# Performance work log

Hardware: AMD Instinct MI355X
Metric: run time of the kernel (lower is better)

Reference implementation:

```python
import jax, jax.numpy as jnp
import numpy as np

N = 100000          # nodes
E = 3200000         # edges
C_IN = 64
HIDDEN = 64
NUM_CLASSES = 10
NUM_GRAPHS = 256
EPS = 1e-5


def _graph_conv(x, src, dst, w_rel, w_root, b):
    # PyG GraphConv(aggr='mean'): out_i = W_rel * mean_{j->i} x_j + W_root * x_i + b
    msg_sum = jax.ops.segment_sum(x[src], dst, num_segments=N)            # [N, C]
    cnt = jax.ops.segment_sum(jnp.ones((src.shape[0], 1), x.dtype), dst,
                              num_segments=N)                             # [N, 1]
    agg = msg_sum / jnp.maximum(cnt, 1.0)
    return agg @ w_rel + x @ w_root + b


def _batch_norm(x, gamma, beta):
    # PyG BatchNorm in training mode: batch stats over the node dimension
    mean = jnp.mean(x, axis=0)
    var = jnp.var(x, axis=0)
    return (x - mean) * jax.lax.rsqrt(var + EPS) * gamma + beta


def setup_inputs() -> dict:
    key = jax.random.key(0)
    ks = jax.random.split(key, 20)
    x = jax.random.normal(ks[0], (N, C_IN), dtype=jnp.float32)
    edge_index = jax.random.randint(ks[1], (2, E), 0, N, dtype=jnp.int32)
    batch = jnp.sort(jax.random.randint(ks[2], (N,), 0, NUM_GRAPHS, dtype=jnp.int32))

    def lin(k, fan_in, fan_out):
        s = 1.0 / np.sqrt(fan_in)
        return jax.random.uniform(k, (fan_in, fan_out), jnp.float32, -s, s)

    dims = [(C_IN, 16), (16, 32), (32, 32), (32, HIDDEN)]
    params = {}
    ki = 3
    for i, (ci, co) in enumerate(dims, start=1):
        params[f"w_rel{i}"] = lin(ks[ki], ci, co); ki += 1
        params[f"w_root{i}"] = lin(ks[ki], ci, co); ki += 1
        params[f"b{i}"] = jnp.zeros((co,), jnp.float32)
        params[f"g{i}"] = jnp.ones((co,), jnp.float32)
        params[f"be{i}"] = jnp.zeros((co,), jnp.float32)
    params["w_lin1"] = lin(ks[ki], HIDDEN, HIDDEN); ki += 1
    params["b_lin1"] = jnp.zeros((HIDDEN,), jnp.float32)
    params["w_lin2"] = lin(ks[ki], HIDDEN, NUM_CLASSES); ki += 1
    params["b_lin2"] = jnp.zeros((NUM_CLASSES,), jnp.float32)

    return {"x": x, "edge_index": edge_index, "batch": batch, **params}


def reference(x, edge_index, batch,
              w_rel1, w_root1, b1, g1, be1,
              w_rel2, w_root2, b2, g2, be2,
              w_rel3, w_root3, b3, g3, be3,
              w_rel4, w_root4, b4, g4, be4,
              w_lin1, b_lin1, w_lin2, b_lin2):
    src, dst = edge_index[0], edge_index[1]
    h = jax.nn.elu(_batch_norm(_graph_conv(x, src, dst, w_rel1, w_root1, b1), g1, be1))
    h = jax.nn.elu(_batch_norm(_graph_conv(h, src, dst, w_rel2, w_root2, b2), g2, be2))
    h = jax.nn.elu(_batch_norm(_graph_conv(h, src, dst, w_rel3, w_root3, b3), g3, be3))
    h = jax.nn.elu(_batch_norm(_graph_conv(h, src, dst, w_rel4, w_root4, b4), g4, be4))
    # global mean pool over graphs
    pooled = jax.ops.segment_sum(h, batch, num_segments=NUM_GRAPHS)
    cnt = jax.ops.segment_sum(jnp.ones((N, 1), h.dtype), batch, num_segments=NUM_GRAPHS)
    pooled = pooled / jnp.maximum(cnt, 1.0)
    z = jax.nn.relu(pooled @ w_lin1 + b_lin1)
    # dropout omitted (deterministic / eval mode)
    logits = z @ w_lin2 + b_lin2
    return jax.nn.log_softmax(logits, axis=-1)
```

## Files before the change

### kernel.cpp

```cpp
#include <hip/hip_runtime.h>
#include <hip/hip_bf16.h>
#include <math.h>

#define NGRAPHS 256
#define BSHIFT 7
#define NBUCK 1024
#define NSORT 64
#define SBLK 256
#define SMASK 0x01FFFFFFu

__global__ __launch_bounds__(1024) void k_bhist(const int* __restrict__ dst, int* __restrict__ hmat, int E) {
    __shared__ int hist[NBUCK];
    for (int i = threadIdx.x; i < NBUCK; i += 1024) hist[i] = 0;
    __syncthreads();
    int chunk = (E + NSORT - 1) / NSORT;
    int lo = blockIdx.x * chunk;
    int hi = lo + chunk; if (hi > E) hi = E;
    for (int i = lo + threadIdx.x; i < hi; i += 1024) {
        int d = __builtin_nontemporal_load(dst + i);
        atomicAdd(&hist[d >> BSHIFT], 1);
    }
    __syncthreads();
    for (int i = threadIdx.x; i < NBUCK; i += 1024)
        hmat[(size_t)blockIdx.x * NBUCK + i] = hist[i];
}

__global__ __launch_bounds__(256) void k_cscan(int* __restrict__ hmat, int* __restrict__ btot) {
    int col = blockIdx.x * 256 + threadIdx.x;
    int run = 0;
#pragma unroll 4
    for (int r = 0; r < NSORT; r++) {
        int v = hmat[(size_t)r * NBUCK + col];
        hmat[(size_t)r * NBUCK + col] = run;
        run += v;
    }
    btot[col] = run;
}

__global__ __launch_bounds__(1024) void k_bscan(const int* __restrict__ btot, int* __restrict__ bstart) {
    __shared__ int s[1024];
    int tid = threadIdx.x;
    int v = btot[tid];
    s[tid] = v;
    __syncthreads();
    for (int off = 1; off < 1024; off <<= 1) {
        int t = (tid >= off) ? s[tid - off] : 0;
        __syncthreads();
        s[tid] += t;
        __syncthreads();
    }
    bstart[tid] = s[tid] - v;
    if (tid == 1023) bstart[NBUCK] = s[1023];
}

__global__ __launch_bounds__(1024) void k_bscatter(const int* __restrict__ src, const int* __restrict__ dst,
                                                   const int* __restrict__ hmat, const int* __restrict__ bstart,
                                                   unsigned* __restrict__ ebuf, int E) {
    __shared__ int cur[NBUCK];
    for (int i = threadIdx.x; i < NBUCK; i += 1024)
        cur[i] = bstart[i] + hmat[(size_t)blockIdx.x * NBUCK + i];
    __syncthreads();
    int chunk = (E + NSORT - 1) / NSORT;
    int lo = blockIdx.x * chunk;
    int hi = lo + chunk; if (hi > E) hi = E;
    for (int i = lo + threadIdx.x; i < hi; i += 1024) {
        int d = __builtin_nontemporal_load(dst + i);
        int s = __builtin_nontemporal_load(src + i);
        int p = atomicAdd(&cur[d >> BSHIFT], 1);
        ebuf[p] = (unsigned)s | ((unsigned)(d & 127) << 25);
    }
}

__global__ __launch_bounds__(256) void k_sort2(const unsigned* __restrict__ ebuf, const int* __restrict__ bstart,
                                               int* __restrict__ csr, int* __restrict__ row_start, int N) {
    __shared__ int hist[128];
    __shared__ int sc[128];
    __shared__ int scur[128];
    int b = blockIdx.x;
    int e0 = bstart[b], e1 = bstart[b + 1];
    if (threadIdx.x < 128) hist[threadIdx.x] = 0;
    __syncthreads();
    for (int i = e0 + threadIdx.x; i < e1; i += 256)
        atomicAdd(&hist[__builtin_nontemporal_load(ebuf + i) >> 25], 1);
    __syncthreads();
    if (threadIdx.x < 128) sc[threadIdx.x] = hist[threadIdx.x];
    __syncthreads();
    for (int off = 1; off < 128; off <<= 1) {
        int t = 0;
        if (threadIdx.x < 128 && threadIdx.x >= off) t = sc[threadIdx.x - off];
        __syncthreads();
        if (threadIdx.x < 128) sc[threadIdx.x] += t;
        __syncthreads();
    }
    if (threadIdx.x < 128) {
        int inc = sc[threadIdx.x];
        int ex = inc - hist[threadIdx.x];
        scur[threadIdx.x] = e0 + ex;
        int node = (b << BSHIFT) + threadIdx.x;
        if (node < N) row_start[node] = e0 + ex;
        if (node == N - 1) row_start[N] = e0 + inc;
    }
    __syncthreads();
    for (int i = e0 + threadIdx.x; i < e1; i += 256) {
        unsigned w = __builtin_nontemporal_load(ebuf + i);
        int p = atomicAdd(&scur[w >> 25], 1);
        csr[p] = (int)(w & SMASK);
    }
}

template <int CI, int CO, bool HAS_REL, bool HAS_ROOT, bool ADD_AGG, bool HAS_BIAS>
__global__ __launch_bounds__(256) void k_lin(const float* __restrict__ hroot, const float* __restrict__ hrel,
                                             const float* __restrict__ w_rel, const float* __restrict__ w_root,
                                             const float* __restrict__ bias, const float* __restrict__ aggadd,
                                             float* __restrict__ out, int N) {
    constexpr int QPR = CO / 4;
    __shared__ float s_rel[HAS_REL ? CI * CO : 1];
    __shared__ float s_root[HAS_ROOT ? CI * CO : 1];
    __shared__ float s_b[HAS_BIAS ? CO : 4];
    if (HAS_REL)
        for (int i = threadIdx.x; i < CI * CO; i += 256) s_rel[i] = w_rel[i];
    if (HAS_ROOT)
        for (int i = threadIdx.x; i < CI * CO; i += 256) s_root[i] = w_root[i];
    if (HAS_BIAS && threadIdx.x < CO) s_b[threadIdx.x] = bias[threadIdx.x];
    __syncthreads();

    int t = blockIdx.x * 256 + threadIdx.x;
    int n = t / QPR;
    int c0 = (t % QPR) * 4;
    if (n >= N) return;

    float rr[HAS_ROOT ? CI : 1];
    if (HAS_ROOT) {
        const float4* hp = (const float4*)(hroot + (size_t)n * CI);
#pragma unroll
        for (int i = 0; i < CI / 4; i++) {
            float4 v = hp[i];
            rr[4 * i + 0] = v.x; rr[4 * i + 1] = v.y; rr[4 * i + 2] = v.z; rr[4 * i + 3] = v.w;
        }
    }
    float ar[HAS_REL ? CI : 1];
    if (HAS_REL) {
        const float4* mp = (const float4*)(hrel + (size_t)n * CI);
#pragma unroll
        for (int i = 0; i < CI / 4; i++) {
            float4 v = mp[i];
            ar[4 * i + 0] = v.x; ar[4 * i + 1] = v.y; ar[4 * i + 2] = v.z; ar[4 * i + 3] = v.w;
        }
    }

    float4 acc;
    if (HAS_BIAS) acc = *(const float4*)&s_b[c0];
    else { acc.x = 0.f; acc.y = 0.f; acc.z = 0.f; acc.w = 0.f; }
    if (ADD_AGG) {
        float4 v = *(const float4*)(aggadd + (size_t)n * CO + c0);
        acc.x += v.x; acc.y += v.y; acc.z += v.z; acc.w += v.w;
    }

#pragma unroll
    for (int ci = 0; ci < CI; ci++) {
        if (HAS_REL) {
            float a = ar[ci];
            float4 w = *(const float4*)&s_rel[ci * CO + c0];
            acc.x += a * w.x; acc.y += a * w.y; acc.z += a * w.z; acc.w += a * w.w;
        }
        if (HAS_ROOT) {
            float hv = rr[ci];
            float4 w = *(const float4*)&s_root[ci * CO + c0];
            acc.x += hv * w.x; acc.y += hv * w.y; acc.z += hv * w.z; acc.w += hv * w.w;
        }
    }
    *(float4*)(out + (size_t)n * CO + c0) = acc;
}

template <int C>
__global__ __launch_bounds__(256) void k_gather(const float* __restrict__ h, const int* __restrict__ row_start,
                                                const int* __restrict__ csr, float* __restrict__ agg, int N) {
    constexpr int LPR = C / 4;
    constexpr int EPP = 64 / LPR;
    int lane = threadIdx.x & 63;
    int wid = blockIdx.x * 4 + (threadIdx.x >> 6);
    if (wid >= N) return;
    int r0 = row_start[wid];
    int deg = row_start[wid + 1] - r0;
    int es = lane / LPR;
    int cq = (lane % LPR) * 4;
    float ax = 0.f, ay = 0.f, az = 0.f, aw = 0.f;
    for (int j0 = 0; j0 < deg; j0 += 4 * EPP) {
        int s[4]; bool p[4];
#pragma unroll
        for (int u = 0; u < 4; u++) {
            int j = j0 + u * EPP + es;
            p[u] = j < deg;
            s[u] = __builtin_nontemporal_load(&csr[r0 + (p[u] ? j : 0)]);
        }
#pragma unroll
        for (int u = 0; u < 4; u++) {
            float4 v = *(const float4*)(h + (size_t)s[u] * C + cq);
            if (p[u]) { ax += v.x; ay += v.y; az += v.z; aw += v.w; }
        }
    }
#pragma unroll
    for (int off = LPR; off < 64; off <<= 1) {
        ax += __shfl_xor(ax, off, 64);
        ay += __shfl_xor(ay, off, 64);
        az += __shfl_xor(az, off, 64);
        aw += __shfl_xor(aw, off, 64);
    }
    if (lane < LPR) {
        float rec = 1.0f / (float)(deg > 0 ? deg : 1);
        float4 o; o.x = ax * rec; o.y = ay * rec; o.z = az * rec; o.w = aw * rec;
        *(float4*)(agg + (size_t)wid * C + cq) = o;
    }
}

template <int CO>
__global__ __launch_bounds__(256) void k_stats(const float* __restrict__ h, float* __restrict__ partials, int N) {
    constexpr int QPR = CO / 4;
    int total = N * QPR;
    float s0 = 0, s1 = 0, s2 = 0, s3 = 0, q0 = 0, q1 = 0, q2 = 0, q3 = 0;
    int idx = blockIdx.x * 256 + threadIdx.x;
    for (int i = idx; i < total; i += SBLK * 256) {
        float4 v = ((const float4*)h)[i];
        s0 += v.x; q0 += v.x * v.x;
        s1 += v.y; q1 += v.y * v.y;
        s2 += v.z; q2 += v.z * v.z;
        s3 += v.w; q3 += v.w * v.w;
    }
#pragma unroll
    for (int off = QPR; off < 64; off <<= 1) {
        s0 += __shfl_xor(s0, off, 64); q0 += __shfl_xor(q0, off, 64);
        s1 += __shfl_xor(s1, off, 64); q1 += __shfl_xor(q1, off, 64);
        s2 += __shfl_xor(s2, off, 64); q2 += __shfl_xor(q2, off, 64);
        s3 += __shfl_xor(s3, off, 64); q3 += __shfl_xor(q3, off, 64);
    }
    __shared__ float part[4][2 * CO];
    int lane = threadIdx.x & 63;
    int w = threadIdx.x >> 6;
    if (lane < QPR) {
        int cq = lane * 4;
        part[w][cq + 0] = s0; part[w][CO + cq + 0] = q0;
        part[w][cq + 1] = s1; part[w][CO + cq + 1] = q1;
        part[w][cq + 2] = s2; part[w][CO + cq + 2] = q2;
        part[w][cq + 3] = s3; part[w][CO + cq + 3] = q3;
    }
    __syncthreads();
    if (threadIdx.x < 2 * CO) {
        float v = part[0][threadIdx.x] + part[1][threadIdx.x] + part[2][threadIdx.x] + part[3][threadIdx.x];
        partials[blockIdx.x * (2 * CO) + threadIdx.x] = v;
    }
}

__global__ __launch_bounds__(128) void k_sfinal(const float* __restrict__ partials, const float* __restrict__ g,
                                                const float* __restrict__ be, float* __restrict__ stats,
                                                int CO, float invN) {
    __shared__ float red[128];
    int c = threadIdx.x;
    float s = 0.f;
    if (c < 2 * CO) {
        for (int b = 0; b < SBLK; b++) s += partials[b * 2 * CO + c];
    }
    red[c] = s;
    __syncthreads();
    if (c < CO) {
        float mean = red[c] * invN;
        float var = red[CO + c] * invN - mean * mean;
        float sc = g[c] * rsqrtf(var + 1e-5f);
        stats[128 + c] = sc;
        stats[192 + c] = be[c] - mean * sc;
    }
}

template <int CO>
__global__ __launch_bounds__(256) void k_bn_elu(float* __restrict__ h, const float* __restrict__ stats, int N) {
    __shared__ float sc[CO], sh[CO];
    if (threadIdx.x < CO) {
        sc[threadIdx.x] = stats[128 + threadIdx.x];
        sh[threadIdx.x] = stats[192 + threadIdx.x];
    }
    __syncthreads();
    int total = N * (CO / 4);
    int i = blockIdx.x * 256 + threadIdx.x;
    if (i >= total) return;
    float4 v = ((float4*)h)[i];
    int cq = (i % (CO / 4)) * 4;
    v.x = v.x * sc[cq + 0] + sh[cq + 0];
    v.y = v.y * sc[cq + 1] + sh[cq + 1];
    v.z = v.z * sc[cq + 2] + sh[cq + 2];
    v.w = v.w * sc[cq + 3] + sh[cq + 3];
    v.x = v.x > 0.f ? v.x : expm1f(v.x);
    v.y = v.y > 0.f ? v.y : expm1f(v.y);
    v.z = v.z > 0.f ? v.z : expm1f(v.z);
    v.w = v.w > 0.f ? v.w : expm1f(v.w);
    ((float4*)h)[i] = v;
}

__global__ __launch_bounds__(256) void k_pool(const float* __restrict__ h, const int* __restrict__ batch,
                                              float* __restrict__ pooled, float* __restrict__ cntg, int N) {
    int lane = threadIdx.x & 63;
    int wid = blockIdx.x * 4 + (threadIdx.x >> 6);
    int n0 = wid * 64;
    if (n0 >= N) return;
    int nmax = N - n0; if (nmax > 64) nmax = 64;
    int cur = batch[n0];
    float acc = 0.f;
    int run = 0;
    for (int k = 0; k < nmax; k++) {
        int g = batch[n0 + k];
        if (g != cur) {
            atomicAdd(&pooled[(size_t)cur * 64 + lane], acc);
            if (lane == 0) atomicAdd(&cntg[cur], (float)run);
            cur = g; acc = 0.f; run = 0;
        }
        acc += h[(size_t)(n0 + k) * 64 + lane];
        run++;
    }
    atomicAdd(&pooled[(size_t)cur * 64 + lane], acc);
    if (lane == 0) atomicAdd(&cntg[cur], (float)run);
}

__global__ __launch_bounds__(256) void k_head(const float* __restrict__ pooled, const float* __restrict__ cntg,
                                              const float* __restrict__ w1, const float* __restrict__ b1,
                                              const float* __restrict__ w2, const float* __restrict__ b2,
                                              float* __restrict__ out) {
    int g = threadIdx.x;
    float rec = 1.0f / fmaxf(cntg[g], 1.0f);
    float p[64];
    {
        const float4* pp = (const float4*)(pooled + (size_t)g * 64);
#pragma unroll
        for (int i = 0; i < 16; i++) {
            float4 v = pp[i];
            p[4 * i + 0] = v.x * rec; p[4 * i + 1] = v.y * rec;
            p[4 * i + 2] = v.z * rec; p[4 * i + 3] = v.w * rec;
        }
    }
    float lg[10];
#pragma unroll
    for (int t = 0; t < 10; t++) lg[t] = b2[t];
#pragma unroll 1
    for (int j = 0; j < 64; j++) {
        float a = b1[j];
#pragma unroll
        for (int k = 0; k < 64; k++) a += p[k] * w1[k * 64 + j];
        a = fmaxf(a, 0.f);
#pragma unroll
        for (int t = 0; t < 10; t++) lg[t] += a * w2[j * 10 + t];
    }
    float m = -1e30f;
#pragma unroll
    for (int t = 0; t < 10; t++) m = fmaxf(m, lg[t]);
    float s = 0.f;
#pragma unroll
    for (int t = 0; t < 10; t++) s += expf(lg[t] - m);
    float lse = m + logf(s);
#pragma unroll
    for (int t = 0; t < 10; t++) out[(size_t)g * 10 + t] = lg[t] - lse;
}

extern "C" void kernel_launch(void* const* d_in, const int* in_sizes, int n_in,
                              void* d_out, int out_size, void* d_ws, size_t ws_size,
                              hipStream_t stream) {
    const float* x = (const float*)d_in[0];
    const int* ei = (const int*)d_in[1];
    const int* batch = (const int*)d_in[2];
    const int N = in_sizes[0] / 64;
    const int E = in_sizes[1] / 2;
    const int* src = ei;
    const int* dst = ei + E;

    const float* w_rel1 = (const float*)d_in[3];
    const float* w_root1 = (const float*)d_in[4];
    const float* b1 = (const float*)d_in[5];
    const float* g1 = (const float*)d_in[6];
    const float* be1 = (const float*)d_in[7];
    const float* w_rel2 = (const float*)d_in[8];
    const float* w_root2 = (const float*)d_in[9];
    const float* b2 = (const float*)d_in[10];
    const float* g2 = (const float*)d_in[11];
    const float* be2 = (const float*)d_in[12];
    const float* w_rel3 = (const float*)d_in[13];
    const float* w_root3 = (const float*)d_in[14];
    const float* b3 = (const float*)d_in[15];
    const float* g3 = (const float*)d_in[16];
    const float* be3 = (const float*)d_in[17];
    const float* w_rel4 = (const float*)d_in[18];
    const float* w_root4 = (const float*)d_in[19];
    const float* b4 = (const float*)d_in[20];
    const float* g4 = (const float*)d_in[21];
    const float* be4 = (const float*)d_in[22];
    const float* w_lin1 = (const float*)d_in[23];
    const float* b_lin1 = (const float*)d_in[24];
    const float* w_lin2 = (const float*)d_in[25];
    const float* b_lin2 = (const float*)d_in[26];

    char* ws = (char*)d_ws;
    size_t off = 0;
    auto alloc = [&](size_t bytes) { size_t o = off; off += (bytes + 255) & ~(size_t)255; return o; };
    int* hmat = (int*)(ws + alloc((size_t)NSORT * NBUCK * 4));
    int* btot = (int*)(ws + alloc((size_t)NBUCK * 4));
    int* bstart = (int*)(ws + alloc((size_t)(NBUCK + 1) * 4));
    unsigned* ebuf = (unsigned*)(ws + alloc((size_t)E * 4));
    int* csr = (int*)(ws + alloc((size_t)E * 4));
    int* row_start = (int*)(ws + alloc((size_t)(N + 1) * 4));
    float* agg = (float*)(ws + alloc((size_t)N * 32 * 4));
    float* y1 = (float*)(ws + alloc((size_t)N * 16 * 4));
    float* bufA = (float*)(ws + alloc((size_t)N * 64 * 4));
    float* bufB = (float*)(ws + alloc((size_t)N * 64 * 4));
    float* stats = (float*)(ws + alloc(4 * 256 * 4));
    float* partials = (float*)(ws + alloc((size_t)SBLK * 128 * 4));
    float* pooled = (float*)(ws + alloc((size_t)(NGRAPHS * 64 + NGRAPHS) * 4));
    float* cntg = pooled + NGRAPHS * 64;

    hipMemsetAsync(pooled, 0, (size_t)(NGRAPHS * 64 + NGRAPHS) * 4, stream);

    const float invN = 1.0f / (float)N;
    const int gbl = (N + 3) / 4;
    auto lgrid = [&](int qpr) { return (N * qpr + 255) / 256; };

    k_bhist<<<NSORT, 1024, 0, stream>>>(dst, hmat, E);
    k_cscan<<<NBUCK / 256, 256, 0, stream>>>(hmat, btot);
    k_bscan<<<1, 1024, 0, stream>>>(btot, bstart);
    k_bscatter<<<NSORT, 1024, 0, stream>>>(src, dst, hmat, bstart, ebuf, E);
    k_sort2<<<NBUCK, 256, 0, stream>>>(ebuf, bstart, csr, row_start, N);

    k_lin<64, 16, true, false, false, false><<<lgrid(4), 256, 0, stream>>>(
        nullptr, x, w_rel1, nullptr, nullptr, nullptr, y1, N);
    k_gather<16><<<gbl, 256, 0, stream>>>(y1, row_start, csr, agg, N);
    k_lin<64, 16, false, true, true, true><<<lgrid(4), 256, 0, stream>>>(
        x, nullptr, nullptr, w_root1, b1, agg, bufA, N);
    k_stats<16><<<SBLK, 256, 0, stream>>>(bufA, partials, N);
    k_sfinal<<<1, 128, 0, stream>>>(partials, g1, be1, stats + 0, 16, invN);
    k_bn_elu<16><<<(N * 4 + 255) / 256, 256, 0, stream>>>(bufA, stats + 0, N);

    k_gather<16><<<gbl, 256, 0, stream>>>(bufA, row_start, csr, agg, N);
    k_lin<16, 32, true, true, false, true><<<lgrid(8), 256, 0, stream>>>(
        bufA, agg, w_rel2, w_root2, b2, nullptr, bufB, N);
    k_stats<32><<<SBLK, 256, 0, stream>>>(bufB, partials, N);
    k_sfinal<<<1, 128, 0, stream>>>(partials, g2, be2, stats + 256, 32, invN);
    k_bn_elu<32><<<(N * 8 + 255) / 256, 256, 0, stream>>>(bufB, stats + 256, N);

    k_gather<32><<<gbl, 256, 0, stream>>>(bufB, row_start, csr, agg, N);
    k_lin<32, 32, true, true, false, true><<<lgrid(8), 256, 0, stream>>>(
        bufB, agg, w_rel3, w_root3, b3, nullptr, bufA, N);
    k_stats<32><<<SBLK, 256, 0, stream>>>(bufA, partials, N);
    k_sfinal<<<1, 128, 0, stream>>>(partials, g3, be3, stats + 512, 32, invN);
    k_bn_elu<32><<<(N * 8 + 255) / 256, 256, 0, stream>>>(bufA, stats + 512, N);

    k_gather<32><<<gbl, 256, 0, stream>>>(bufA, row_start, csr, agg, N);
    k_lin<32, 64, true, true, false, true><<<lgrid(16), 256, 0, stream>>>(
        bufA, agg, w_rel4, w_root4, b4, nullptr, bufB, N);
    k_stats<64><<<SBLK, 256, 0, stream>>>(bufB, partials, N);
    k_sfinal<<<1, 128, 0, stream>>>(partials, g4, be4, stats + 768, 64, invN);
    k_bn_elu<64><<<(N * 16 + 255) / 256, 256, 0, stream>>>(bufB, stats + 768, N);

    int waves = (N + 63) / 64;
    k_pool<<<(waves + 3) / 4, 256, 0, stream>>>(bufB, batch, pooled, cntg, N);
    k_head<<<1, 256, 0, stream>>>(pooled, cntg, w_lin1, b_lin1, w_lin2, b_lin2, (float*)d_out);
}
```

Before: 661.6 us.

## Fuse BatchNorm statistics into linear kernels and retune sort block config

Computes per-channel sum and sum-of-squares inside k_lin epilogues and writes per-block partials. This removes the separate k_stats pass that re-read each layer output. A new two-stage reduction (k_sred, then k_sfinal) replaces the single-block reduction over partials, so more partials are written and one small launch is added per layer. Separately, the edge-sort histogram and scatter kernels now use 128 blocks of 256 threads instead of 64 blocks of 1024.

```diff
diff --git a/kernel.cpp b/kernel.cpp
--- a/kernel.cpp
+++ b/kernel.cpp
@@ -5,23 +5,22 @@
 #define NGRAPHS 256
 #define BSHIFT 7
 #define NBUCK 1024
-#define NSORT 64
-#define SBLK 256
+#define NSORT 128
 #define SMASK 0x01FFFFFFu
 
-__global__ __launch_bounds__(1024) void k_bhist(const int* __restrict__ dst, int* __restrict__ hmat, int E) {
+__global__ __launch_bounds__(256) void k_bhist(const int* __restrict__ dst, int* __restrict__ hmat, int E) {
     __shared__ int hist[NBUCK];
-    for (int i = threadIdx.x; i < NBUCK; i += 1024) hist[i] = 0;
+    for (int i = threadIdx.x; i < NBUCK; i += 256) hist[i] = 0;
     __syncthreads();
     int chunk = (E + NSORT - 1) / NSORT;
     int lo = blockIdx.x * chunk;
     int hi = lo + chunk; if (hi > E) hi = E;
-    for (int i = lo + threadIdx.x; i < hi; i += 1024) {
+    for (int i = lo + threadIdx.x; i < hi; i += 256) {
         int d = __builtin_nontemporal_load(dst + i);
         atomicAdd(&hist[d >> BSHIFT], 1);
     }
     __syncthreads();
-    for (int i = threadIdx.x; i < NBUCK; i += 1024)
+    for (int i = threadIdx.x; i < NBUCK; i += 256)
         hmat[(size_t)blockIdx.x * NBUCK + i] = hist[i];
 }
 
@@ -53,17 +52,17 @@
     if (tid == 1023) bstart[NBUCK] = s[1023];
 }
 
-__global__ __launch_bounds__(1024) void k_bscatter(const int* __restrict__ src, const int* __restrict__ dst,
-                                                   const int* __restrict__ hmat, const int* __restrict__ bstart,
-                                                   unsigned* __restrict__ ebuf, int E) {
+__global__ __launch_bounds__(256) void k_bscatter(const int* __restrict__ src, const int* __restrict__ dst,
+                                                  const int* __restrict__ hmat, const int* __restrict__ bstart,
+                                                  unsigned* __restrict__ ebuf, int E) {
     __shared__ int cur[NBUCK];
-    for (int i = threadIdx.x; i < NBUCK; i += 1024)
+    for (int i = threadIdx.x; i < NBUCK; i += 256)
         cur[i] = bstart[i] + hmat[(size_t)blockIdx.x * NBUCK + i];
     __syncthreads();
     int chunk = (E + NSORT - 1) / NSORT;
     int lo = blockIdx.x * chunk;
     int hi = lo + chunk; if (hi > E) hi = E;
-    for (int i = lo + threadIdx.x; i < hi; i += 1024) {
+    for (int i = lo + threadIdx.x; i < hi; i += 256) {
         int d = __builtin_nontemporal_load(dst + i);
         int s = __builtin_nontemporal_load(src + i);
         int p = atomicAdd(&cur[d >> BSHIFT], 1);
@@ -108,11 +107,11 @@
     }
 }
 
-template <int CI, int CO, bool HAS_REL, bool HAS_ROOT, bool ADD_AGG, bool HAS_BIAS>
+template <int CI, int CO, bool HAS_REL, bool HAS_ROOT, bool ADD_AGG, bool HAS_BIAS, bool STATS>
 __global__ __launch_bounds__(256) void k_lin(const float* __restrict__ hroot, const float* __restrict__ hrel,
                                              const float* __restrict__ w_rel, const float* __restrict__ w_root,
                                              const float* __restrict__ bias, const float* __restrict__ aggadd,
-                                             float* __restrict__ out, int N) {
+                                             float* __restrict__ out, float* __restrict__ partials, int N) {
     constexpr int QPR = CO / 4;
     __shared__ float s_rel[HAS_REL ? CI * CO : 1];
     __shared__ float s_root[HAS_ROOT ? CI * CO : 1];
@@ -127,11 +126,12 @@
     int t = blockIdx.x * 256 + threadIdx.x;
     int n = t / QPR;
     int c0 = (t % QPR) * 4;
-    if (n >= N) return;
+    bool valid = n < N;
+    int nn = valid ? n : 0;
 
     float rr[HAS_ROOT ? CI : 1];
     if (HAS_ROOT) {
-        const float4* hp = (const float4*)(hroot + (size_t)n * CI);
+        const float4* hp = (const float4*)(hroot + (size_t)nn * CI);
 #pragma unroll
         for (int i = 0; i < CI / 4; i++) {
             float4 v = hp[i];
@@ -140,7 +140,7 @@
     }
     float ar[HAS_REL ? CI : 1];
     if (HAS_REL) {
-        const float4* mp = (const float4*)(hrel + (size_t)n * CI);
+        const float4* mp = (const float4*)(hrel + (size_t)nn * CI);
 #pragma unroll
         for (int i = 0; i < CI / 4; i++) {
             float4 v = mp[i];
@@ -152,7 +152,7 @@
     if (HAS_BIAS) acc = *(const float4*)&s_b[c0];
     else { acc.x = 0.f; acc.y = 0.f; acc.z = 0.f; acc.w = 0.f; }
     if (ADD_AGG) {
-        float4 v = *(const float4*)(aggadd + (size_t)n * CO + c0);
+        float4 v = *(const float4*)(aggadd + (size_t)nn * CO + c0);
         acc.x += v.x; acc.y += v.y; acc.z += v.z; acc.w += v.w;
     }
 
@@ -169,7 +169,64 @@
             acc.x += hv * w.x; acc.y += hv * w.y; acc.z += hv * w.z; acc.w += hv * w.w;
         }
     }
-    *(float4*)(out + (size_t)n * CO + c0) = acc;
+    if (valid) *(float4*)(out + (size_t)n * CO + c0) = acc;
+
+    if (STATS) {
+        float s0 = valid ? acc.x : 0.f, s1 = valid ? acc.y : 0.f;
+        float s2 = valid ? acc.z : 0.f, s3 = valid ? acc.w : 0.f;
+        float q0 = s0 * s0, q1 = s1 * s1, q2 = s2 * s2, q3 = s3 * s3;
+#pragma unroll
+        for (int off = QPR; off < 64; off <<= 1) {
+            s0 += __shfl_xor(s0, off, 64); q0 += __shfl_xor(q0, off, 64);
+            s1 += __shfl_xor(s1, off, 64); q1 += __shfl_xor(q1, off, 64);
+            s2 += __shfl_xor(s2, off, 64); q2 += __shfl_xor(q2, off, 64);
+            s3 += __shfl_xor(s3, off, 64); q3 += __shfl_xor(q3, off, 64);
+        }
+        __shared__ float part[4][2 * CO];
+        int lane = threadIdx.x & 63;
+        int w = threadIdx.x >> 6;
+        if (lane < QPR) {
+            int cq = lane * 4;
+            part[w][cq + 0] = s0; part[w][CO + cq + 0] = q0;
+            part[w][cq + 1] = s1; part[w][CO + cq + 1] = q1;
+            part[w][cq + 2] = s2; part[w][CO + cq + 2] = q2;
+            part[w][cq + 3] = s3; part[w][CO + cq + 3] = q3;
+        }
+        __syncthreads();
+        if (threadIdx.x < 2 * CO) {
+            float v = part[0][threadIdx.x] + part[1][threadIdx.x] + part[2][threadIdx.x] + part[3][threadIdx.x];
+            partials[(size_t)blockIdx.x * (2 * CO) + threadIdx.x] = v;
+        }
+    }
+}
+
+__global__ __launch_bounds__(128) void k_sred(const float* __restrict__ partials, float* __restrict__ pred,
+                                              int twoCO, int nb) {
+    int c = threadIdx.x;
+    if (c >= twoCO) return;
+    float s = 0.f;
+    for (int b = blockIdx.x; b < nb; b += 64) s += partials[(size_t)b * twoCO + c];
+    pred[(size_t)blockIdx.x * twoCO + c] = s;
+}
+
+__global__ __launch_bounds__(128) void k_sfinal(const float* __restrict__ pred, const float* __restrict__ g,
+                                                const float* __restrict__ be, float* __restrict__ stats,
+                                                int CO, float invN) {
+    __shared__ float red[128];
+    int c = threadIdx.x;
+    float s = 0.f;
+    if (c < 2 * CO) {
+        for (int b = 0; b < 64; b++) s += pred[(size_t)b * 2 * CO + c];
+    }
+    red[c] = s;
+    __syncthreads();
+    if (c < CO) {
+        float mean = red[c] * invN;
+        float var = red[CO + c] * invN - mean * mean;
+        float sc = g[c] * rsqrtf(var + 1e-5f);
+        stats[128 + c] = sc;
+        stats[192 + c] = be[c] - mean * sc;
+    }
 }
 
 template <int C>
@@ -210,63 +267,6 @@
         float rec = 1.0f / (float)(deg > 0 ? deg : 1);
         float4 o; o.x = ax * rec; o.y = ay * rec; o.z = az * rec; o.w = aw * rec;
         *(float4*)(agg + (size_t)wid * C + cq) = o;
-    }
-}
-
-template <int CO>
-__global__ __launch_bounds__(256) void k_stats(const float* __restrict__ h, float* __restrict__ partials, int N) {
-    constexpr int QPR = CO / 4;
-    int total = N * QPR;
-    float s0 = 0, s1 = 0, s2 = 0, s3 = 0, q0 = 0, q1 = 0, q2 = 0, q3 = 0;
-    int idx = blockIdx.x * 256 + threadIdx.x;
-    for (int i = idx; i < total; i += SBLK * 256) {
-        float4 v = ((const float4*)h)[i];
-        s0 += v.x; q0 += v.x * v.x;
-        s1 += v.y; q1 += v.y * v.y;
-        s2 += v.z; q2 += v.z * v.z;
-        s3 += v.w; q3 += v.w * v.w;
-    }
-#pragma unroll
-    for (int off = QPR; off < 64; off <<= 1) {
-        s0 += __shfl_xor(s0, off, 64); q0 += __shfl_xor(q0, off, 64);
-        s1 += __shfl_xor(s1, off, 64); q1 += __shfl_xor(q1, off, 64);
-        s2 += __shfl_xor(s2, off, 64); q2 += __shfl_xor(q2, off, 64);
-        s3 += __shfl_xor(s3, off, 64); q3 += __shfl_xor(q3, off, 64);
-    }
-    __shared__ float part[4][2 * CO];
-    int lane = threadIdx.x & 63;
-    int w = threadIdx.x >> 6;
-    if (lane < QPR) {
-        int cq = lane * 4;
-        part[w][cq + 0] = s0; part[w][CO + cq + 0] = q0;
-        part[w][cq + 1] = s1; part[w][CO + cq + 1] = q1;
-        part[w][cq + 2] = s2; part[w][CO + cq + 2] = q2;
-        part[w][cq + 3] = s3; part[w][CO + cq + 3] = q3;
-    }
-    __syncthreads();
-    if (threadIdx.x < 2 * CO) {
-        float v = part[0][threadIdx.x] + part[1][threadIdx.x] + part[2][threadIdx.x] + part[3][threadIdx.x];
-        partials[blockIdx.x * (2 * CO) + threadIdx.x] = v;
-    }
-}
-
-__global__ __launch_bounds__(128) void k_sfinal(const float* __restrict__ partials, const float* __restrict__ g,
-                                                const float* __restrict__ be, float* __restrict__ stats,
-                                                int CO, float invN) {
-    __shared__ float red[128];
-    int c = threadIdx.x;
-    float s = 0.f;
-    if (c < 2 * CO) {
-        for (int b = 0; b < SBLK; b++) s += partials[b * 2 * CO + c];
-    }
-    red[c] = s;
-    __syncthreads();
-    if (c < CO) {
-        float mean = red[c] * invN;
-        float var = red[CO + c] * invN - mean * mean;
-        float sc = g[c] * rsqrtf(var + 1e-5f);
-        stats[128 + c] = sc;
-        stats[192 + c] = be[c] - mean * sc;
     }
 }
 
@@ -407,7 +407,11 @@
     float* bufA = (float*)(ws + alloc((size_t)N * 64 * 4));
     float* bufB = (float*)(ws + alloc((size_t)N * 64 * 4));
     float* stats = (float*)(ws + alloc(4 * 256 * 4));
-    float* partials = (float*)(ws + alloc((size_t)SBLK * 128 * 4));
+    const int nb16 = (N * 4 + 255) / 256;
+    const int nb32 = (N * 8 + 255) / 256;
+    const int nb64 = (N * 16 + 255) / 256;
+    float* partials = (float*)(ws + alloc((size_t)nb64 * 128 * 4));
+    float* pred = (float*)(ws + alloc((size_t)64 * 128 * 4));
     float* pooled = (float*)(ws + alloc((size_t)(NGRAPHS * 64 + NGRAPHS) * 4));
     float* cntg = pooled + NGRAPHS * 64;
 
@@ -415,42 +419,41 @@
 
     const float invN = 1.0f / (float)N;
     const int gbl = (N + 3) / 4;
-    auto lgrid = [&](int qpr) { return (N * qpr + 255) / 256; };
-
-    k_bhist<<<NSORT, 1024, 0, stream>>>(dst, hmat, E);
+
+    k_bhist<<<NSORT, 256, 0, stream>>>(dst, hmat, E);
     k_cscan<<<NBUCK / 256, 256, 0, stream>>>(hmat, btot);
     k_bscan<<<1, 1024, 0, stream>>>(btot, bstart);
-    k_bscatter<<<NSORT, 1024, 0, stream>>>(src, dst, hmat, bstart, ebuf, E);
+    k_bscatter<<<NSORT, 256, 0, stream>>>(src, dst, hmat, bstart, ebuf, E);
     k_sort2<<<NBUCK, 256, 0, stream>>>(ebuf, bstart, csr, row_start, N);
 
-    k_lin<64, 16, true, false, false, false><<<lgrid(4), 256, 0, stream>>>(
-        nullptr, x, w_rel1, nullptr, nullptr, nullptr, y1, N);
+    k_lin<64, 16, true, false, false, false, false><<<nb16, 256, 0, stream>>>(
+        nullptr, x, w_rel1, nullptr, nullptr, nullptr, y1, nullptr, N);
     k_gather<16><<<gbl, 256, 0, stream>>>(y1, row_start, csr, agg, N);
-    k_lin<64, 16, false, true, true, true><<<lgrid(4), 256, 0, stream>>>(
-        x, nullptr, nullptr, w_root1, b1, agg, bufA, N);
-    k_stats<16><<<SBLK, 256, 0, stream>>>(bufA, partials, N);
-    k_sfinal<<<1, 128, 0, stream>>>(partials, g1, be1, stats + 0, 16, invN);
+    k_lin<64, 16, false, true, true, true, true><<<nb16, 256, 0, stream>>>(
+        x, nullptr, nullptr, w_root1, b1, agg, bufA, partials, N);
+    k_sred<<<64, 128, 0, stream>>>(partials, pred, 32, nb16);
+    k_sfinal<<<1, 128, 0, stream>>>(pred, g1, be1, stats + 0, 16, invN);
     k_bn_elu<16><<<(N * 4 + 255) / 256, 256, 0, stream>>>(bufA, stats + 0, N);
 
     k_gather<16><<<gbl, 256, 0, stream>>>(bufA, row_start, csr, agg, N);
-    k_lin<16, 32, true, true, false, true><<<lgrid(8), 256, 0, stream>>>(
-        bufA, agg, w_rel2, w_root2, b2, nullptr, bufB, N);
-    k_stats<32><<<SBLK, 256, 0, stream>>>(bufB, partials, N);
-    k_sfinal<<<1, 128, 0, stream>>>(partials, g2, be2, stats + 256, 32, invN);
+    k_lin<16, 32, true, true, false, true, true><<<nb32, 256, 0, stream>>>(
+        bufA, agg, w_rel2, w_root2, b2, nullptr, bufB, partials, N);
+    k_sred<<<64, 128, 0, stream>>>(partials, pred, 64, nb32);
+    k_sfinal<<<1, 128, 0, stream>>>(pred, g2, be2, stats + 256, 32, invN);
     k_bn_elu<32><<<(N * 8 + 255) / 256, 256, 0, stream>>>(bufB, stats + 256, N);
 
     k_gather<32><<<gbl, 256, 0, stream>>>(bufB, row_start, csr, agg, N);
-    k_lin<32, 32, true, true, false, true><<<lgrid(8), 256, 0, stream>>>(
-        bufB, agg, w_rel3, w_root3, b3, nullptr, bufA, N);
-    k_stats<32><<<SBLK, 256, 0, stream>>>(bufA, partials, N);
-    k_sfinal<<<1, 128, 0, stream>>>(partials, g3, be3, stats + 512, 32, invN);
+    k_lin<32, 32, true, true, false, true, true><<<nb32, 256, 0, stream>>>(
+        bufB, agg, w_rel3, w_root3, b3, nullptr, bufA, partials, N);
+    k_sred<<<64, 128, 0, stream>>>(partials, pred, 64, nb32);
+    k_sfinal<<<1, 128, 0, stream>>>(pred, g3, be3, stats + 512, 32, invN);
     k_bn_elu<32><<<(N * 8 + 255) / 256, 256, 0, stream>>>(bufA, stats + 512, N);
 
     k_gather<32><<<gbl, 256, 0, stream>>>(bufA, row_start, csr, agg, N);
-    k_lin<32, 64, true, true, false, true><<<lgrid(16), 256, 0, stream>>>(
-        bufA, agg, w_rel4, w_root4, b4, nullptr, bufB, N);
-    k_stats<64><<<SBLK, 256, 0, stream>>>(bufB, partials, N);
-    k_sfinal<<<1, 128, 0, stream>>>(partials, g4, be4, stats + 768, 64, invN);
+    k_lin<32, 64, true, true, false, true, true><<<nb64, 256, 0, stream>>>(
+        bufA, agg, w_rel4, w_root4, b4, nullptr, bufB, partials, N);
+    k_sred<<<64, 128, 0, stream>>>(partials, pred, 128, nb64);
+    k_sfinal<<<1, 128, 0, stream>>>(pred, g4, be4, stats + 768, 64, invN);
     k_bn_elu<64><<<(N * 16 + 255) / 256, 256, 0, stream>>>(bufB, stats + 768, N);
 
     int waves = (N + 63) / 64;
```

Result: slower. 702.6 us (+6.2%).
